# Performance work log

Hardware: AMD Instinct MI355X
Metric: run time of the kernel (lower is better)

The kernel has to match this reference:

```python
import jax, jax.numpy as jnp
import numpy as np
import math

DIM = 1024
MLP = 4096
D_STATE = 16
D_CONV = 4
EXPAND = 2
D_INNER = EXPAND * DIM
HALF = D_INNER // 2
DT_RANK = math.ceil(DIM / 16)
BSZ = 2
SEQ = 2048
LN_EPS = 1e-5


def setup_inputs() -> dict:
    key = jax.random.key(0)
    ks = jax.random.split(key, 12)
    s = lambda k, shape, sc: jax.random.normal(k, shape, dtype=jnp.float32) * sc
    return {
        "x": s(ks[0], (BSZ, SEQ, DIM), 1.0),
        "ln1_g": jnp.ones((DIM,), jnp.float32),
        "ln1_b": jnp.zeros((DIM,), jnp.float32),
        "in_proj_w": s(ks[1], (D_INNER, DIM), 0.02),
        "conv_x_w": s(ks[2], (HALF, 1, D_CONV), 0.1),
        "conv_x_b": jnp.zeros((HALF,), jnp.float32),
        "conv_z_w": s(ks[3], (HALF, 1, D_CONV), 0.1),
        "conv_z_b": jnp.zeros((HALF,), jnp.float32),
        "x_proj_w": s(ks[4], (DT_RANK + 2 * D_STATE, HALF), 0.02),
        "dt_proj_w": s(ks[5], (HALF, DT_RANK), 0.02),
        "dt_proj_b": s(ks[6], (HALF,), 0.1),
        "A_log": jnp.log(jnp.tile(jnp.arange(1, D_STATE + 1, dtype=jnp.float32), (HALF, 1))),
        "Dp": jnp.ones((HALF,), jnp.float32),
        "out_proj_w": s(ks[7], (DIM, D_INNER), 0.02),
        "ln2_g": jnp.ones((DIM,), jnp.float32),
        "ln2_b": jnp.zeros((DIM,), jnp.float32),
        "mlp_w1": s(ks[8], (MLP, DIM), 0.02),
        "mlp_b1": jnp.zeros((MLP,), jnp.float32),
        "mlp_w2": s(ks[9], (DIM, MLP), 0.02),
        "mlp_b2": jnp.zeros((DIM,), jnp.float32),
    }


def _ln(x, g, b):
    mu = jnp.mean(x, -1, keepdims=True)
    v = jnp.mean((x - mu) ** 2, -1, keepdims=True)
    return (x - mu) * jax.lax.rsqrt(v + LN_EPS) * g + b


def _dwconv_same(x, w, b):
    # x: [B, C, L]; w: [C, 1, K] depthwise; PyTorch 'same' pads left=(K-1)//2, right=rest
    total = D_CONV - 1
    left = total // 2
    y = jax.lax.conv_general_dilated(
        x, w, (1,), [(left, total - left)],
        dimension_numbers=("NCH", "OIH", "NCH"),
        feature_group_count=x.shape[1])
    return y + b[None, :, None]


def _mixer(x, in_proj_w, conv_x_w, conv_x_b, conv_z_w, conv_z_b,
           x_proj_w, dt_proj_w, dt_proj_b, A_log, Dp, out_proj_w):
    Bsz = x.shape[0]
    xz = jnp.einsum('bld,ed->ble', x, in_proj_w)              # [B,L,2*HALF]
    xs, zs = jnp.split(xz, 2, axis=-1)
    xc = jax.nn.silu(_dwconv_same(jnp.swapaxes(xs, 1, 2), conv_x_w, conv_x_b))  # [B,HALF,L]
    zc = jax.nn.silu(_dwconv_same(jnp.swapaxes(zs, 1, 2), conv_z_w, conv_z_b))  # [B,HALF,L]
    u = jnp.swapaxes(xc, 1, 2)                                 # [B,L,HALF]
    x_dbl = jnp.einsum('bld,ed->ble', u, x_proj_w)             # [B,L,dt_rank+2N]
    dt, Bm, Cm = jnp.split(x_dbl, [DT_RANK, DT_RANK + D_STATE], axis=-1)
    delta = jax.nn.softplus(jnp.einsum('blr,dr->bld', dt, dt_proj_w) + dt_proj_b)  # [B,L,HALF]
    A = -jnp.exp(A_log)                                        # [HALF,N]
    dA = jnp.exp(jnp.einsum('bld,dn->lbdn', delta, A))         # [L,B,HALF,N]
    dBu = jnp.einsum('bld,bln,bld->lbdn', delta, Bm, u)        # [L,B,HALF,N]
    Cs = jnp.moveaxis(Cm, 1, 0)                                # [L,B,N]

    def step(h, t):
        dA_t, dBu_t, c_t = t
        h = dA_t * h + dBu_t                                   # [B,HALF,N]
        return h, jnp.einsum('bdn,bn->bd', h, c_t)

    h0 = jnp.zeros((Bsz, HALF, D_STATE), x.dtype)
    _, ys = jax.lax.scan(step, h0, (dA, dBu, Cs))              # ys: [L,B,HALF]
    y = jnp.moveaxis(ys, 0, 1) + u * Dp                        # [B,L,HALF]
    y = jnp.concatenate([y, jnp.swapaxes(zc, 1, 2)], axis=-1)  # [B,L,2*HALF]
    return jnp.einsum('ble,de->bld', y, out_proj_w)


def reference(x, ln1_g, ln1_b, in_proj_w, conv_x_w, conv_x_b, conv_z_w, conv_z_b,
              x_proj_w, dt_proj_w, dt_proj_b, A_log, Dp, out_proj_w,
              ln2_g, ln2_b, mlp_w1, mlp_b1, mlp_w2, mlp_b2):
    x = x + _mixer(_ln(x, ln1_g, ln1_b), in_proj_w, conv_x_w, conv_x_b,
                   conv_z_w, conv_z_b, x_proj_w, dt_proj_w, dt_proj_b,
                   A_log, Dp, out_proj_w)
    h = _ln(x, ln2_g, ln2_b)
    h = jax.nn.gelu(jnp.einsum('bld,md->blm', h, mlp_w1) + mlp_b1, approximate=False)
    h = jnp.einsum('blm,dm->bld', h, mlp_w2) + mlp_b2
    return x + h
```

## Files before the change

kernel.cpp:

```cpp
#include <hip/hip_runtime.h>
#include <math.h>

#define DIMD    1024
#define MLPD    4096
#define DSTATE  16
#define DCONV   4
#define HALF    1024
#define DINNER  2048
#define DTRANK  64
#define BSZ     2
#define SEQ     2048
#define NTOK    (BSZ*SEQ)
#define NCH     64
#define CL      (SEQ/NCH)

typedef short bf16x8 __attribute__((ext_vector_type(8)));
typedef float f32x4  __attribute__((ext_vector_type(4)));
typedef unsigned short u16;
typedef unsigned int   u32;

__device__ __forceinline__ u16 f2bf(float x) {
    union { float f; unsigned int u; } v; v.f = x;
    unsigned int r = (v.u + 0x7FFFu + ((v.u >> 16) & 1u)) >> 16;
    return (u16)r;
}
__device__ __forceinline__ float bf2f(u16 x) {
    union { unsigned int u; float f; } v; v.u = ((unsigned int)x) << 16;
    return v.f;
}

#define SZ_WIN  (DINNER*DIMD)
#define SZ_WXP  (96*HALF)
#define SZ_WDT  (HALF*DTRANK)
#define SZ_WOUT (DIMD*DINNER)
#define SZ_WM1  (MLPD*DIMD)
#define SZ_WM2  (DIMD*MLPD)
#define SZ_TOT  (SZ_WIN+SZ_WXP+SZ_WDT+SZ_WOUT+SZ_WM1+SZ_WM2)

__global__ __launch_bounds__(256) void cvt6_kernel(
        const float* __restrict__ s0, u16* __restrict__ d0,
        const float* __restrict__ s1, u16* __restrict__ d1,
        const float* __restrict__ s2, u16* __restrict__ d2,
        const float* __restrict__ s3, u16* __restrict__ d3,
        const float* __restrict__ s4, u16* __restrict__ d4,
        const float* __restrict__ s5, u16* __restrict__ d5) {
    int i = blockIdx.x * 256 + threadIdx.x;
    if (i < SZ_WIN)  { d0[i] = f2bf(s0[i]); return; }  i -= SZ_WIN;
    if (i < SZ_WXP)  { d1[i] = f2bf(s1[i]); return; }  i -= SZ_WXP;
    if (i < SZ_WDT)  { d2[i] = f2bf(s2[i]); return; }  i -= SZ_WDT;
    if (i < SZ_WOUT) { d3[i] = f2bf(s3[i]); return; }  i -= SZ_WOUT;
    if (i < SZ_WM1)  { d4[i] = f2bf(s4[i]); return; }  i -= SZ_WM1;
    d5[i] = f2bf(s5[i]);
}

__global__ __launch_bounds__(256) void ln_bf16_kernel(
        const float* __restrict__ x, const float* __restrict__ g,
        const float* __restrict__ b, u16* __restrict__ out) {
    __shared__ float sm[4];
    int row = blockIdx.x;
    int t = threadIdx.x;
    const float4* xr = (const float4*)(x + (size_t)row * DIMD);
    float4 v = xr[t];
    float s = v.x + v.y + v.z + v.w;
    for (int off = 32; off > 0; off >>= 1) s += __shfl_down(s, off, 64);
    if ((t & 63) == 0) sm[t >> 6] = s;
    __syncthreads();
    float mu = (sm[0] + sm[1] + sm[2] + sm[3]) * (1.0f / DIMD);
    float dx = v.x - mu, dy = v.y - mu, dz = v.z - mu, dw = v.w - mu;
    float ss = dx*dx + dy*dy + dz*dz + dw*dw;
    for (int off = 32; off > 0; off >>= 1) ss += __shfl_down(ss, off, 64);
    __syncthreads();
    if ((t & 63) == 0) sm[t >> 6] = ss;
    __syncthreads();
    float var = (sm[0] + sm[1] + sm[2] + sm[3]) * (1.0f / DIMD);
    float rs = rsqrtf(var + 1e-5f);
    float4 gv = ((const float4*)g)[t];
    float4 bv = ((const float4*)b)[t];
    u16* o = out + (size_t)row * DIMD + t * 4;
    o[0] = f2bf(dx * rs * gv.x + bv.x);
    o[1] = f2bf(dy * rs * gv.y + bv.y);
    o[2] = f2bf(dz * rs * gv.z + bv.z);
    o[3] = f2bf(dw * rs * gv.w + bv.w);
}

__global__ __launch_bounds__(64) void gemm_small_kernel(
        const u16* __restrict__ A, int lda,
        const u16* __restrict__ W, int K, int N,
        float* __restrict__ Cf, u16* __restrict__ Cb) {
    int m0 = blockIdx.x * 16;
    int n0 = blockIdx.y * 16;
    int lane = threadIdx.x;
    int r = lane & 15, quad = lane >> 4;
    f32x4 acc = {0.f, 0.f, 0.f, 0.f};
    const u16* ap = A + (size_t)(m0 + r) * lda + quad * 8;
    const u16* wp = W + (size_t)(n0 + r) * K   + quad * 8;
    for (int k = 0; k < K; k += 32) {
        bf16x8 av = *(const bf16x8*)(ap + k);
        bf16x8 bv = *(const bf16x8*)(wp + k);
        acc = __builtin_amdgcn_mfma_f32_16x16x32_bf16(av, bv, acc, 0, 0, 0);
    }
    int col = n0 + r;
    #pragma unroll
    for (int i = 0; i < 4; ++i) {
        int row = m0 + quad * 4 + i;
        size_t idx = (size_t)row * N + col;
        Cf[idx] = acc[i];
        Cb[idx] = f2bf(acc[i]);
    }
}

template<int EPI, int TN>
__global__ __launch_bounds__(256) void gemm128_kernel(
        const u16* __restrict__ A, int lda, const u16* __restrict__ W,
        int K, int N,
        const float* __restrict__ bias, const float* __restrict__ resid,
        float* __restrict__ Cf, u16* __restrict__ Cb) {
    constexpr int NF = TN / 32;
    __shared__ u16 As[2][128 * 32];
    __shared__ u16 Bs[2][TN * 32];
    const int t = threadIdx.x;
    const int w = t >> 6;
    const int lane = t & 63;
    const int r = lane & 15, quad = lane >> 4;
    const int wm = w & 1, wn = w >> 1;
    const int m0 = blockIdx.x * 128;
    const int n0 = blockIdx.y * TN;

    f32x4 acc[4][NF];
    #pragma unroll
    for (int mi = 0; mi < 4; ++mi)
        #pragma unroll
        for (int ni = 0; ni < NF; ++ni)
            acc[mi][ni] = (f32x4){0.f, 0.f, 0.f, 0.f};

    auto stage = [&](int buf, int k0) {
        #pragma unroll
        for (int i = 0; i < 2; ++i) {
            int c = (i * 4 + w) * 64 + lane;
            int row = c >> 2;
            int q = (c & 3) ^ ((row >> 1) & 3);
            const u16* ga = A + (size_t)(m0 + row) * lda + k0 + q * 8;
            __builtin_amdgcn_global_load_lds(
                (const __attribute__((address_space(1))) u32*)ga,
                (__attribute__((address_space(3))) u32*)(As[buf] + (i * 4 + w) * 512),
                16, 0, 0);
        }
        #pragma unroll
        for (int i = 0; i < NF / 2; ++i) {
            int c = (i * 4 + w) * 64 + lane;
            int row = c >> 2;
            int q = (c & 3) ^ ((row >> 1) & 3);
            const u16* gb = W + (size_t)(n0 + row) * K + k0 + q * 8;
            __builtin_amdgcn_global_load_lds(
                (const __attribute__((address_space(1))) u32*)gb,
                (__attribute__((address_space(3))) u32*)(Bs[buf] + (i * 4 + w) * 512),
                16, 0, 0);
        }
    };

    stage(0, 0);
    int cur = 0;
    for (int k0 = 0; k0 < K; k0 += 32, cur ^= 1) {
        __syncthreads();
        if (k0 + 32 < K) stage(cur ^ 1, k0 + 32);
        const int qs = quad ^ ((r >> 1) & 3);
        bf16x8 af[4], bfr[NF];
        #pragma unroll
        for (int mi = 0; mi < 4; ++mi) {
            int row = wm * 64 + mi * 16 + r;
            af[mi] = *(const bf16x8*)&As[cur][row * 32 + qs * 8];
        }
        #pragma unroll
        for (int ni = 0; ni < NF; ++ni) {
            int row = wn * (TN / 2) + ni * 16 + r;
            bfr[ni] = *(const bf16x8*)&Bs[cur][row * 32 + qs * 8];
        }
        #pragma unroll
        for (int mi = 0; mi < 4; ++mi)
            #pragma unroll
            for (int ni = 0; ni < NF; ++ni)
                acc[mi][ni] = __builtin_amdgcn_mfma_f32_16x16x32_bf16(
                    af[mi], bfr[ni], acc[mi][ni], 0, 0, 0);
    }
    #pragma unroll
    for (int mi = 0; mi < 4; ++mi) {
        #pragma unroll
        for (int i = 0; i < 4; ++i) {
            int row = m0 + wm * 64 + mi * 16 + quad * 4 + i;
            #pragma unroll
            for (int ni = 0; ni < NF; ++ni) {
                int col = n0 + wn * (TN / 2) + ni * 16 + r;
                size_t idx = (size_t)row * N + col;
                float v = acc[mi][ni][i];
                if (EPI == 1) { v += bias[col]; v = (v > 20.f) ? v : log1pf(expf(v)); }
                if (EPI == 2) { v += bias[col]; v = 0.5f * v * (1.0f + erff(v * 0.70710678118654752f)); }
                if (EPI == 3) { v += resid[idx]; }
                if (EPI == 4) { v += bias[col] + resid[idx]; }
                if (EPI == 2 || EPI == 5) Cb[idx] = f2bf(v);
                else                      Cf[idx] = v;
            }
        }
    }
}

__global__ __launch_bounds__(256) void conv_silu_kernel(
        const u16* __restrict__ xz,
        const float* __restrict__ wx, const float* __restrict__ bx,
        const float* __restrict__ wz, const float* __restrict__ bz,
        u16* __restrict__ u_bf, u16* __restrict__ ycat) {
    int c  = blockIdx.x * 256 + threadIdx.x;
    int bl = blockIdx.y;
    int l  = bl & (SEQ - 1);
    float accx = bx[c], accz = bz[c];
    #pragma unroll
    for (int k = 0; k < DCONV; ++k) {
        int lp = l + k - 1;
        if (lp >= 0 && lp < SEQ) {
            const u16* rowp = xz + (size_t)(bl + (lp - l)) * DINNER;
            accx += bf2f(rowp[c])        * wx[c * DCONV + k];
            accz += bf2f(rowp[HALF + c]) * wz[c * DCONV + k];
        }
    }
    float sx = accx * __fdividef(1.f, 1.f + __expf(-accx));
    float sz = accz * __fdividef(1.f, 1.f + __expf(-accz));
    u_bf[(size_t)bl * HALF + c] = f2bf(sx);
    ycat[(size_t)bl * DINNER + HALF + c] = f2bf(sz);
}

__global__ __launch_bounds__(256) void scan_p1_kernel(
        const float* __restrict__ delta, const u16* __restrict__ u_bf,
        const float* __restrict__ x_dbl, const float* __restrict__ A_log,
        float* __restrict__ hfin, float* __restrict__ dsum) {
    int t  = blockIdx.x * 256 + threadIdx.x;
    int d  = t & (HALF - 1);
    int ch = (t >> 10) & (NCH - 1);
    int b  = t >> 16;
    float Ac[16], h[16];
    #pragma unroll
    for (int i = 0; i < 4; ++i) {
        float4 a = *(const float4*)&A_log[d * DSTATE + i * 4];
        Ac[4*i+0] = -__expf(a.x); Ac[4*i+1] = -__expf(a.y);
        Ac[4*i+2] = -__expf(a.z); Ac[4*i+3] = -__expf(a.w);
        h[4*i+0] = 0.f; h[4*i+1] = 0.f; h[4*i+2] = 0.f; h[4*i+3] = 0.f;
    }
    int l0 = b * SEQ + ch * CL;
    size_t off = (size_t)l0 * HALF + d;
    const float* xrow = x_dbl + (size_t)l0 * 96;
    float ds = 0.f;
    #pragma unroll 4
    for (int l = 0; l < CL; ++l) {
        float dl = delta[off];
        float uv = bf2f(u_bf[off]);
        off += HALF;
        float4 B0 = *(const float4*)(xrow + 64);
        float4 B1 = *(const float4*)(xrow + 68);
        float4 B2 = *(const float4*)(xrow + 72);
        float4 B3 = *(const float4*)(xrow + 76);
        xrow += 96;
        float dBu = dl * uv;
        ds += dl;
        float Bv[16] = {B0.x,B0.y,B0.z,B0.w, B1.x,B1.y,B1.z,B1.w,
                        B2.x,B2.y,B2.z,B2.w, B3.x,B3.y,B3.z,B3.w};
        #pragma unroll
        for (int n = 0; n < 16; ++n)
            h[n] = __expf(dl * Ac[n]) * h[n] + dBu * Bv[n];
    }
    float4* hf = (float4*)&hfin[(size_t)t * 16];
    #pragma unroll
    for (int i = 0; i < 4; ++i)
        hf[i] = (float4){h[4*i+0], h[4*i+1], h[4*i+2], h[4*i+3]};
    dsum[t] = ds;
}

__global__ __launch_bounds__(256) void scan_p2_kernel(
        const float* __restrict__ A_log, const float* __restrict__ dsum,
        const float* __restrict__ hfin, float* __restrict__ hin) {
    int t = blockIdx.x * 256 + threadIdx.x;
    int n = t & 15;
    int d = (t >> 4) & (HALF - 1);
    int b = t >> 14;
    float Ac = -__expf(A_log[d * DSTATE + n]);
    float h = 0.f;
    for (int ch = 0; ch < NCH; ++ch) {
        size_t chain = ((size_t)(b * NCH + ch) * HALF) + d;
        hin[chain * 16 + n] = h;
        float ds = dsum[chain];
        h = __expf(Ac * ds) * h + hfin[chain * 16 + n];
    }
}

__global__ __launch_bounds__(256) void scan_p3_kernel(
        const float* __restrict__ delta, const u16* __restrict__ u_bf,
        const float* __restrict__ x_dbl, const float* __restrict__ A_log,
        const float* __restrict__ Dp, const float* __restrict__ hin,
        u16* __restrict__ ycat) {
    int t  = blockIdx.x * 256 + threadIdx.x;
    int d  = t & (HALF - 1);
    int ch = (t >> 10) & (NCH - 1);
    int b  = t >> 16;
    float Ac[16], h[16];
    #pragma unroll
    for (int i = 0; i < 4; ++i) {
        float4 a  = *(const float4*)&A_log[d * DSTATE + i * 4];
        float4 hv = *(const float4*)&hin[(size_t)t * 16 + i * 4];
        Ac[4*i+0] = -__expf(a.x); Ac[4*i+1] = -__expf(a.y);
        Ac[4*i+2] = -__expf(a.z); Ac[4*i+3] = -__expf(a.w);
        h[4*i+0] = hv.x; h[4*i+1] = hv.y; h[4*i+2] = hv.z; h[4*i+3] = hv.w;
    }
    float Dv = Dp[d];
    int l0 = b * SEQ + ch * CL;
    size_t off = (size_t)l0 * HALF + d;
    const float* xrow = x_dbl + (size_t)l0 * 96;
    u16* yp = ycat + (size_t)l0 * DINNER + d;
    #pragma unroll 4
    for (int l = 0; l < CL; ++l) {
        float dl = delta[off];
        float uv = bf2f(u_bf[off]);
        off += HALF;
        float4 B0 = *(const float4*)(xrow + 64);
        float4 B1 = *(const float4*)(xrow + 68);
        float4 B2 = *(const float4*)(xrow + 72);
        float4 B3 = *(const float4*)(xrow + 76);
        float4 C0 = *(const float4*)(xrow + 80);
        float4 C1 = *(const float4*)(xrow + 84);
        float4 C2 = *(const float4*)(xrow + 88);
        float4 C3 = *(const float4*)(xrow + 92);
        xrow += 96;
        float dBu = dl * uv;
        float Bv[16] = {B0.x,B0.y,B0.z,B0.w, B1.x,B1.y,B1.z,B1.w,
                        B2.x,B2.y,B2.z,B2.w, B3.x,B3.y,B3.z,B3.w};
        float Cv[16] = {C0.x,C0.y,C0.z,C0.w, C1.x,C1.y,C1.z,C1.w,
                        C2.x,C2.y,C2.z,C2.w, C3.x,C3.y,C3.z,C3.w};
        float y = uv * Dv;
        #pragma unroll
        for (int n = 0; n < 16; ++n) {
            h[n] = __expf(dl * Ac[n]) * h[n] + dBu * Bv[n];
            y += h[n] * Cv[n];
        }
        *yp = f2bf(y);
        yp += DINNER;
    }
}

extern "C" void kernel_launch(void* const* d_in, const int* in_sizes, int n_in,
                              void* d_out, int out_size, void* d_ws, size_t ws_size,
                              hipStream_t stream) {
    const float* x         = (const float*)d_in[0];
    const float* ln1_g     = (const float*)d_in[1];
    const float* ln1_b     = (const float*)d_in[2];
    const float* in_proj_w = (const float*)d_in[3];
    const float* conv_x_w  = (const float*)d_in[4];
    const float* conv_x_b  = (const float*)d_in[5];
    const float* conv_z_w  = (const float*)d_in[6];
    const float* conv_z_b  = (const float*)d_in[7];
    const float* x_proj_w  = (const float*)d_in[8];
    const float* dt_proj_w = (const float*)d_in[9];
    const float* dt_proj_b = (const float*)d_in[10];
    const float* A_log     = (const float*)d_in[11];
    const float* Dp        = (const float*)d_in[12];
    const float* out_proj_w= (const float*)d_in[13];
    const float* ln2_g     = (const float*)d_in[14];
    const float* ln2_b     = (const float*)d_in[15];
    const float* mlp_w1    = (const float*)d_in[16];
    const float* mlp_b1    = (const float*)d_in[17];
    const float* mlp_w2    = (const float*)d_in[18];
    const float* mlp_b2    = (const float*)d_in[19];
    float* out = (float*)d_out;

    char* p = (char*)d_ws;
    auto alloc = [&](size_t bytes) {
        char* r = p; p += (bytes + 255) & ~(size_t)255; return r;
    };
    u16*   w_in   = (u16*)  alloc((size_t)DINNER * DIMD * 2);
    u16*   w_xp   = (u16*)  alloc((size_t)96 * HALF * 2);
    u16*   w_dt   = (u16*)  alloc((size_t)HALF * DTRANK * 2);
    u16*   w_out  = (u16*)  alloc((size_t)DIMD * DINNER * 2);
    u16*   w_m1   = (u16*)  alloc((size_t)MLPD * DIMD * 2);
    u16*   w_m2   = (u16*)  alloc((size_t)DIMD * MLPD * 2);
    u16*   xn_bf  = (u16*)  alloc((size_t)NTOK * DIMD * 2);
    u16*   xz_bf  = (u16*)  alloc((size_t)NTOK * DINNER * 2);
    u16*   u_bf   = (u16*)  alloc((size_t)NTOK * HALF * 2);
    u16*   ycat   = (u16*)  alloc((size_t)NTOK * DINNER * 2);
    float* x_dbl  = (float*)alloc((size_t)NTOK * 96 * 4);
    u16*   xdbl_bf= (u16*)  alloc((size_t)NTOK * 96 * 2);
    float* delta  = (float*)alloc((size_t)NTOK * HALF * 4);
    float* x2     = (float*)alloc((size_t)NTOK * DIMD * 4);
    u16*   ln2_bf = (u16*)  alloc((size_t)NTOK * DIMD * 2);
    u16*   mlp_h  = (u16*)  alloc((size_t)NTOK * MLPD * 2);
    float* hfin = (float*)mlp_h;
    float* hin  = hfin + (size_t)BSZ * NCH * HALF * DSTATE;
    float* dsum = hin  + (size_t)BSZ * NCH * HALF * DSTATE;

    cvt6_kernel<<<SZ_TOT / 256, 256, 0, stream>>>(
        in_proj_w, w_in, x_proj_w, w_xp, dt_proj_w, w_dt,
        out_proj_w, w_out, mlp_w1, w_m1, mlp_w2, w_m2);

    ln_bf16_kernel<<<NTOK, 256, 0, stream>>>(x, ln1_g, ln1_b, xn_bf);

    gemm128_kernel<5,128><<<dim3(NTOK/128, DINNER/128), 256, 0, stream>>>(
        xn_bf, DIMD, w_in, DIMD, DINNER, nullptr, nullptr, nullptr, xz_bf);

    conv_silu_kernel<<<dim3(HALF/256, NTOK), 256, 0, stream>>>(
        xz_bf, conv_x_w, conv_x_b, conv_z_w, conv_z_b, u_bf, ycat);

    gemm_small_kernel<<<dim3(NTOK/16, 96/16), 64, 0, stream>>>(
        u_bf, HALF, w_xp, HALF, 96, x_dbl, xdbl_bf);

    gemm128_kernel<1,64><<<dim3(NTOK/128, HALF/64), 256, 0, stream>>>(
        xdbl_bf, 96, w_dt, DTRANK, HALF, dt_proj_b, nullptr, delta, nullptr);

    scan_p1_kernel<<<(BSZ*NCH*HALF)/256, 256, 0, stream>>>(
        delta, u_bf, x_dbl, A_log, hfin, dsum);
    scan_p2_kernel<<<(BSZ*HALF*DSTATE)/256, 256, 0, stream>>>(
        A_log, dsum, hfin, hin);
    scan_p3_kernel<<<(BSZ*NCH*HALF)/256, 256, 0, stream>>>(
        delta, u_bf, x_dbl, A_log, Dp, hin, ycat);

    gemm128_kernel<3,64><<<dim3(NTOK/128, DIMD/64), 256, 0, stream>>>(
        ycat, DINNER, w_out, DINNER, DIMD, nullptr, x, x2, nullptr);

    ln_bf16_kernel<<<NTOK, 256, 0, stream>>>(x2, ln2_g, ln2_b, ln2_bf);

    gemm128_kernel<2,128><<<dim3(NTOK/128, MLPD/128), 256, 0, stream>>>(
        ln2_bf, DIMD, w_m1, DIMD, MLPD, mlp_b1, nullptr, nullptr, mlp_h);

    gemm128_kernel<4,64><<<dim3(NTOK/128, DIMD/64), 256, 0, stream>>>(
        mlp_h, MLPD, w_m2, MLPD, DIMD, mlp_b2, x2, out, nullptr);
}
```

Measured before the change: 491.6 us.

## Split-K the out_proj and MLP-down GEMMs and unroll the double-buffered main loop

The two GEMMs with N=1024 (out_proj, K=2048, and mlp_w2, K=4096) launch only 32x16=512 blocks. They now split K in two across blockIdx.z, write fp32 partials into reused scratch buffers, and a separate vectorized reduce kernel adds the partials, residual and bias. The GEMM main loop is also manually unrolled by two with fixed LDS buffers and precomputed global and LDS address offsets, which cuts per-iteration index arithmetic. The split-K path adds extra fp32 partial traffic and two kernel launches in exchange for more parallelism and shorter per-block K loops.

```diff
diff --git a/kernel.cpp b/kernel.cpp
--- a/kernel.cpp
+++ b/kernel.cpp
@@ -109,15 +109,16 @@
     }
 }
 
-template<int EPI, int TN>
+template<int EPI, int TN, int KS>
 __global__ __launch_bounds__(256) void gemm128_kernel(
         const u16* __restrict__ A, int lda, const u16* __restrict__ W,
         int K, int N,
         const float* __restrict__ bias, const float* __restrict__ resid,
-        float* __restrict__ Cf, u16* __restrict__ Cb) {
+        float* __restrict__ Cf, float* __restrict__ Cf2,
+        u16* __restrict__ Cb) {
     constexpr int NF = TN / 32;
-    __shared__ u16 As[2][128 * 32];
-    __shared__ u16 Bs[2][TN * 32];
+    __shared__ u16 As0[128 * 32], As1[128 * 32];
+    __shared__ u16 Bs0[TN * 32],  Bs1[TN * 32];
     const int t = threadIdx.x;
     const int w = t >> 6;
     const int lane = t & 63;
@@ -125,6 +126,8 @@
     const int wm = w & 1, wn = w >> 1;
     const int m0 = blockIdx.x * 128;
     const int n0 = blockIdx.y * TN;
+    const int Kloc = K / KS;
+    const int kz = (KS == 2) ? blockIdx.z : 0;
 
     f32x4 acc[4][NF];
     #pragma unroll
@@ -133,55 +136,74 @@
         for (int ni = 0; ni < NF; ++ni)
             acc[mi][ni] = (f32x4){0.f, 0.f, 0.f, 0.f};
 
-    auto stage = [&](int buf, int k0) {
+    const u16* pa[2];
+    const u16* pb[NF / 2];
+    #pragma unroll
+    for (int i = 0; i < 2; ++i) {
+        int c = (i * 4 + w) * 64 + lane;
+        int row = c >> 2;
+        int q = (c & 3) ^ ((row >> 1) & 3);
+        pa[i] = A + (size_t)(m0 + row) * lda + (size_t)kz * Kloc + q * 8;
+    }
+    #pragma unroll
+    for (int i = 0; i < NF / 2; ++i) {
+        int c = (i * 4 + w) * 64 + lane;
+        int row = c >> 2;
+        int q = (c & 3) ^ ((row >> 1) & 3);
+        pb[i] = W + (size_t)(n0 + row) * K + (size_t)kz * Kloc + q * 8;
+    }
+    const int qs = quad ^ ((r >> 1) & 3);
+    int aoff[4], boff[NF];
+    #pragma unroll
+    for (int mi = 0; mi < 4; ++mi)
+        aoff[mi] = (wm * 64 + mi * 16 + r) * 32 + qs * 8;
+    #pragma unroll
+    for (int ni = 0; ni < NF; ++ni)
+        boff[ni] = (wn * (TN / 2) + ni * 16 + r) * 32 + qs * 8;
+
+    auto stage = [&](u16* __restrict__ Ad, u16* __restrict__ Bd) {
         #pragma unroll
         for (int i = 0; i < 2; ++i) {
-            int c = (i * 4 + w) * 64 + lane;
-            int row = c >> 2;
-            int q = (c & 3) ^ ((row >> 1) & 3);
-            const u16* ga = A + (size_t)(m0 + row) * lda + k0 + q * 8;
             __builtin_amdgcn_global_load_lds(
-                (const __attribute__((address_space(1))) u32*)ga,
-                (__attribute__((address_space(3))) u32*)(As[buf] + (i * 4 + w) * 512),
+                (const __attribute__((address_space(1))) u32*)pa[i],
+                (__attribute__((address_space(3))) u32*)(Ad + (i * 4 + w) * 512),
                 16, 0, 0);
+            pa[i] += 32;
         }
         #pragma unroll
         for (int i = 0; i < NF / 2; ++i) {
-            int c = (i * 4 + w) * 64 + lane;
-            int row = c >> 2;
-            int q = (c & 3) ^ ((row >> 1) & 3);
-            const u16* gb = W + (size_t)(n0 + row) * K + k0 + q * 8;
             __builtin_amdgcn_global_load_lds(
-                (const __attribute__((address_space(1))) u32*)gb,
-                (__attribute__((address_space(3))) u32*)(Bs[buf] + (i * 4 + w) * 512),
+                (const __attribute__((address_space(1))) u32*)pb[i],
+                (__attribute__((address_space(3))) u32*)(Bd + (i * 4 + w) * 512),
                 16, 0, 0);
+            pb[i] += 32;
         }
     };
-
-    stage(0, 0);
-    int cur = 0;
-    for (int k0 = 0; k0 < K; k0 += 32, cur ^= 1) {
-        __syncthreads();
-        if (k0 + 32 < K) stage(cur ^ 1, k0 + 32);
-        const int qs = quad ^ ((r >> 1) & 3);
+    auto compute = [&](const u16* __restrict__ Ab, const u16* __restrict__ Bb) {
         bf16x8 af[4], bfr[NF];
         #pragma unroll
-        for (int mi = 0; mi < 4; ++mi) {
-            int row = wm * 64 + mi * 16 + r;
-            af[mi] = *(const bf16x8*)&As[cur][row * 32 + qs * 8];
-        }
-        #pragma unroll
-        for (int ni = 0; ni < NF; ++ni) {
-            int row = wn * (TN / 2) + ni * 16 + r;
-            bfr[ni] = *(const bf16x8*)&Bs[cur][row * 32 + qs * 8];
-        }
+        for (int mi = 0; mi < 4; ++mi) af[mi] = *(const bf16x8*)(Ab + aoff[mi]);
+        #pragma unroll
+        for (int ni = 0; ni < NF; ++ni) bfr[ni] = *(const bf16x8*)(Bb + boff[ni]);
         #pragma unroll
         for (int mi = 0; mi < 4; ++mi)
             #pragma unroll
             for (int ni = 0; ni < NF; ++ni)
                 acc[mi][ni] = __builtin_amdgcn_mfma_f32_16x16x32_bf16(
                     af[mi], bfr[ni], acc[mi][ni], 0, 0, 0);
-    }
+    };
+
+    stage(As0, Bs0);
+    for (int k0 = 0; k0 < Kloc; k0 += 64) {
+        __syncthreads();
+        if (k0 + 32 < Kloc) stage(As1, Bs1);
+        compute(As0, Bs0);
+        __syncthreads();
+        if (k0 + 64 < Kloc) stage(As0, Bs0);
+        compute(As1, Bs1);
+    }
+
+    float* Cfo = (KS == 2 && kz) ? Cf2 : Cf;
     #pragma unroll
     for (int mi = 0; mi < 4; ++mi) {
         #pragma unroll
@@ -197,10 +219,32 @@
                 if (EPI == 3) { v += resid[idx]; }
                 if (EPI == 4) { v += bias[col] + resid[idx]; }
                 if (EPI == 2 || EPI == 5) Cb[idx] = f2bf(v);
-                else                      Cf[idx] = v;
+                else                      Cfo[idx] = v;
             }
         }
     }
+}
+
+template<int EPI>
+__global__ __launch_bounds__(256) void reduce2_kernel(
+        const float* __restrict__ P0, const float* __restrict__ P1,
+        const float* __restrict__ bias, const float* __restrict__ resid,
+        float* __restrict__ out) {
+    size_t idx = ((size_t)blockIdx.x * 256 + threadIdx.x) * 4;
+    float4 a = *(const float4*)(P0 + idx);
+    float4 b = *(const float4*)(P1 + idx);
+    float4 rr = *(const float4*)(resid + idx);
+    float4 o;
+    o.x = a.x + b.x + rr.x;
+    o.y = a.y + b.y + rr.y;
+    o.z = a.z + b.z + rr.z;
+    o.w = a.w + b.w + rr.w;
+    if (EPI == 4) {
+        int col = (int)(idx & (DIMD - 1));
+        float4 bb = *(const float4*)(bias + col);
+        o.x += bb.x; o.y += bb.y; o.z += bb.z; o.w += bb.w;
+    }
+    *(float4*)(out + idx) = o;
 }
 
 __global__ __launch_bounds__(256) void conv_silu_kernel(
@@ -390,6 +434,8 @@
     float* hfin = (float*)mlp_h;
     float* hin  = hfin + (size_t)BSZ * NCH * HALF * DSTATE;
     float* dsum = hin  + (size_t)BSZ * NCH * HALF * DSTATE;
+    float* P0 = delta;
+    float* P1 = (float*)xz_bf;
 
     cvt6_kernel<<<SZ_TOT / 256, 256, 0, stream>>>(
         in_proj_w, w_in, x_proj_w, w_xp, dt_proj_w, w_dt,
@@ -397,8 +443,8 @@
 
     ln_bf16_kernel<<<NTOK, 256, 0, stream>>>(x, ln1_g, ln1_b, xn_bf);
 
-    gemm128_kernel<5,128><<<dim3(NTOK/128, DINNER/128), 256, 0, stream>>>(
-        xn_bf, DIMD, w_in, DIMD, DINNER, nullptr, nullptr, nullptr, xz_bf);
+    gemm128_kernel<5,128,1><<<dim3(NTOK/128, DINNER/128), 256, 0, stream>>>(
+        xn_bf, DIMD, w_in, DIMD, DINNER, nullptr, nullptr, nullptr, nullptr, xz_bf);
 
     conv_silu_kernel<<<dim3(HALF/256, NTOK), 256, 0, stream>>>(
         xz_bf, conv_x_w, conv_x_b, conv_z_w, conv_z_b, u_bf, ycat);
@@ -406,8 +452,8 @@
     gemm_small_kernel<<<dim3(NTOK/16, 96/16), 64, 0, stream>>>(
         u_bf, HALF, w_xp, HALF, 96, x_dbl, xdbl_bf);
 
-    gemm128_kernel<1,64><<<dim3(NTOK/128, HALF/64), 256, 0, stream>>>(
-        xdbl_bf, 96, w_dt, DTRANK, HALF, dt_proj_b, nullptr, delta, nullptr);
+    gemm128_kernel<1,64,1><<<dim3(NTOK/128, HALF/64), 256, 0, stream>>>(
+        xdbl_bf, 96, w_dt, DTRANK, HALF, dt_proj_b, nullptr, delta, nullptr, nullptr);
 
     scan_p1_kernel<<<(BSZ*NCH*HALF)/256, 256, 0, stream>>>(
         delta, u_bf, x_dbl, A_log, hfin, dsum);
@@ -416,14 +462,18 @@
     scan_p3_kernel<<<(BSZ*NCH*HALF)/256, 256, 0, stream>>>(
         delta, u_bf, x_dbl, A_log, Dp, hin, ycat);
 
-    gemm128_kernel<3,64><<<dim3(NTOK/128, DIMD/64), 256, 0, stream>>>(
-        ycat, DINNER, w_out, DINNER, DIMD, nullptr, x, x2, nullptr);
+    gemm128_kernel<0,64,2><<<dim3(NTOK/128, DIMD/64, 2), 256, 0, stream>>>(
+        ycat, DINNER, w_out, DINNER, DIMD, nullptr, nullptr, P0, P1, nullptr);
+    reduce2_kernel<3><<<(NTOK*DIMD)/1024, 256, 0, stream>>>(
+        P0, P1, nullptr, x, x2);
 
     ln_bf16_kernel<<<NTOK, 256, 0, stream>>>(x2, ln2_g, ln2_b, ln2_bf);
 
-    gemm128_kernel<2,128><<<dim3(NTOK/128, MLPD/128), 256, 0, stream>>>(
-        ln2_bf, DIMD, w_m1, DIMD, MLPD, mlp_b1, nullptr, nullptr, mlp_h);
-
-    gemm128_kernel<4,64><<<dim3(NTOK/128, DIMD/64), 256, 0, stream>>>(
-        mlp_h, MLPD, w_m2, MLPD, DIMD, mlp_b2, x2, out, nullptr);
-}
+    gemm128_kernel<2,128,1><<<dim3(NTOK/128, MLPD/128), 256, 0, stream>>>(
+        ln2_bf, DIMD, w_m1, DIMD, MLPD, mlp_b1, nullptr, nullptr, nullptr, mlp_h);
+
+    gemm128_kernel<0,64,2><<<dim3(NTOK/128, DIMD/64, 2), 256, 0, stream>>>(
+        mlp_h, MLPD, w_m2, MLPD, DIMD, nullptr, nullptr, P0, P1, nullptr);
+    reduce2_kernel<4><<<(NTOK*DIMD)/1024, 256, 0, stream>>>(
+        P0, P1, mlp_b2, x2, out);
+}
```

After: 480.9 us. -2.2%, faster.
